# Performance work log

Hardware: AMD Instinct MI355X
Metric: run time of the kernel (lower is better)

Reference implementation:

```python
import jax, jax.numpy as jnp
import numpy as np

B, N, D_IN = 256, 64, 128   # batch, n_agents, input_dim
H0, H1, H2 = 256, 256, 64   # rnn_hidden_dim[0], [1], [2]


def setup_inputs() -> dict:
    key = jax.random.key(0)
    ks = jax.random.split(key, 14)
    s = 0.05
    return {
        "obs": jax.random.normal(ks[0], (B, N, D_IN), dtype=jnp.float32),
        "W_enc": jax.random.normal(ks[1], (H0, D_IN), dtype=jnp.float32) * s,
        "b_enc": jax.random.normal(ks[2], (H0,), dtype=jnp.float32) * s,
        "W_obs": jax.random.normal(ks[3], (H0, H0), dtype=jnp.float32) * s,
        "b_obs": jax.random.normal(ks[4], (H0,), dtype=jnp.float32) * s,
        "W_ih": jax.random.normal(ks[5], (3 * H0, H0), dtype=jnp.float32) * s,
        "b_ih": jax.random.normal(ks[6], (3 * H0,), dtype=jnp.float32) * s,
        "W_hh": jax.random.normal(ks[7], (3 * H0, H0), dtype=jnp.float32) * s,
        "b_hh": jax.random.normal(ks[8], (3 * H0,), dtype=jnp.float32) * s,
        "W_val": jax.random.normal(ks[9], (H1, H0), dtype=jnp.float32) * s,
        "b_val": jax.random.normal(ks[10], (H1,), dtype=jnp.float32) * s,
        "W_dec": jax.random.normal(ks[11], (H2, H1), dtype=jnp.float32) * s,
        "b_dec": jax.random.normal(ks[12], (H2,), dtype=jnp.float32) * s,
    }


def reference(obs, W_enc, b_enc, W_obs, b_obs, W_ih, b_ih, W_hh, b_hh,
              W_val, b_val, W_dec, b_dec):
    # encoding + f_obs  -> h: [B, N, H0]
    x = jax.nn.relu(jnp.einsum("bnd,hd->bnh", obs, W_enc) + b_enc)
    h = jnp.einsum("bnh,gh->bng", x, W_obs) + b_obs

    # comm: mean over other agents. Original masks self and divides by N
    # (mean over dim of size N with self zeroed) => (sum_all - self) / N.
    c = (jnp.sum(h, axis=1, keepdims=True) - h) / N  # [B, N, H0]

    # GRUCell(input=c, hidden=h), PyTorch gate ordering r, z, n
    gi = jnp.einsum("bnh,gh->bng", c, W_ih) + b_ih   # [B, N, 3*H0]
    gh = jnp.einsum("bnh,gh->bng", h, W_hh) + b_hh
    gi_r, gi_z, gi_n = jnp.split(gi, 3, axis=-1)
    gh_r, gh_z, gh_n = jnp.split(gh, 3, axis=-1)
    r = jax.nn.sigmoid(gi_r + gh_r)
    z = jax.nn.sigmoid(gi_z + gh_z)
    n = jnp.tanh(gi_n + r * gh_n)
    h = (1.0 - z) * n + z * h  # [B, N, H0]

    # value head + decoding; seq_len=1 squeezed -> [B, N, H2]
    v = jnp.einsum("bnh,vh->bnv", h, W_val) + b_val
    out = jnp.einsum("bnv,ov->bno", v, W_dec) + b_dec
    return out
```

## Files before the change

kernel.cpp:

```cpp
#include <hip/hip_runtime.h>
#include <hip/hip_bf16.h>
#include <math.h>


typedef __bf16  bf16x8 __attribute__((ext_vector_type(8)));
typedef float   f32x4  __attribute__((ext_vector_type(4)));

#define DIN 128
#define H0  256
#define SW  264
#define SWO 136
#define LOG2E 1.44269504088896f

#define O_WENC 0
#define O_WOBS 32768
#define O_WIH  98304
#define O_WHH  294912
#define O_WVAL 491520
#define O_WDEC 557056
#define W_TOT  573440

__device__ __forceinline__ f32x4 mfma16(bf16x8 a, bf16x8 b, f32x4 c) {
    return __builtin_amdgcn_mfma_f32_16x16x32_bf16(a, b, c, 0, 0, 0);
}
__device__ __forceinline__ float bf2f(__hip_bfloat16 x) { return __bfloat162float(x); }
__device__ __forceinline__ __hip_bfloat16 f2bf(float x) { return __float2bfloat16(x); }

__device__ __forceinline__ float fsigmoid(float x) {
    float e = __builtin_amdgcn_exp2f(-LOG2E * x);
    return __builtin_amdgcn_rcpf(1.0f + e);
}
__device__ __forceinline__ float ftanh(float x) {
    float e = __builtin_amdgcn_exp2f(2.0f * LOG2E * x);
    return 1.0f - 2.0f * __builtin_amdgcn_rcpf(1.0f + e);
}

__device__ __forceinline__ bf16x8 w8(const __hip_bfloat16* p, int idx) {
    return *(const bf16x8*)(p + idx);
}

__device__ __forceinline__ int tadr(int r, int k) { return r * SW + k; }
__device__ __forceinline__ int oadr(int r, int k) { return r * SWO + k; }

__global__ __launch_bounds__(256) void prep_kernel(
    const float* __restrict__ W_enc, const float* __restrict__ W_obs,
    const float* __restrict__ W_ih,  const float* __restrict__ W_hh,
    const float* __restrict__ W_val, const float* __restrict__ W_dec,
    __hip_bfloat16* __restrict__ ws)
{
    const int i = (blockIdx.x * 256 + threadIdx.x) * 8;
    if (i >= W_TOT) return;
    const float* src; int off;
    if      (i < O_WOBS) { src = W_enc; off = O_WENC; }
    else if (i < O_WIH)  { src = W_obs; off = O_WOBS; }
    else if (i < O_WHH)  { src = W_ih;  off = O_WIH;  }
    else if (i < O_WVAL) { src = W_hh;  off = O_WHH;  }
    else if (i < O_WDEC) { src = W_val; off = O_WVAL; }
    else                 { src = W_dec; off = O_WDEC; }
    const float* f = src + (i - off);
    f32x4 a = *(const f32x4*)f;
    f32x4 b = *(const f32x4*)(f + 4);
    bf16x8 v;
    #pragma unroll
    for (int j = 0; j < 4; j++) { v[j] = (__bf16)a[j]; v[j + 4] = (__bf16)b[j]; }
    *(bf16x8*)(ws + i) = v;
}

__global__ __launch_bounds__(512, 2) void commnet_mfma(
    const __hip_bfloat16* __restrict__ ws,
    const float* __restrict__ b_enc, const float* __restrict__ b_obs,
    const float* __restrict__ b_ih,  const float* __restrict__ b_hh,
    const float* __restrict__ b_val, const float* __restrict__ b_dec,
    const float* __restrict__ obs,   float* __restrict__ out)
{
    __shared__ __align__(16) __hip_bfloat16 T0[64 * SW];
    __shared__ __align__(16) __hip_bfloat16 T1[64 * SW];

    const __hip_bfloat16* W_enc = ws + O_WENC;
    const __hip_bfloat16* W_obs = ws + O_WOBS;
    const __hip_bfloat16* W_ih  = ws + O_WIH;
    const __hip_bfloat16* W_hh  = ws + O_WHH;
    const __hip_bfloat16* W_val = ws + O_WVAL;
    const __hip_bfloat16* W_dec = ws + O_WDEC;

    const int tid  = threadIdx.x;
    const int wave = tid >> 6;
    const int lane = tid & 63;
    const int quad = lane >> 4;
    const int lc   = lane & 15;
    const int row0 = blockIdx.x * 64;
    const int ko16 = quad * 8;

    for (int i = tid; i < 64 * DIN / 8; i += 512) {
        const int r = i >> 4;
        const int c = (i & 15) << 3;
        const float* src = obs + (row0 + r) * DIN + c;
        f32x4 a = *(const f32x4*)src;
        f32x4 b = *(const f32x4*)(src + 4);
        bf16x8 v;
        #pragma unroll
        for (int j = 0; j < 4; j++) { v[j] = (__bf16)a[j]; v[j + 4] = (__bf16)b[j]; }
        *(bf16x8*)&T1[oadr(r, c)] = v;
    }
    __syncthreads();

    #pragma unroll
    for (int cp = 0; cp < 2; cp++) {
        const int n = (wave + 8 * cp) * 16 + lc;
        const float bias = b_enc[n];
        f32x4 acc[4] = {};
        #pragma unroll
        for (int k0 = 0; k0 < DIN; k0 += 32) {
            const int kk = k0 + ko16;
            bf16x8 b = w8(W_enc, n * DIN + kk);
            #pragma unroll
            for (int rt = 0; rt < 4; rt++) {
                bf16x8 a = *(const bf16x8*)&T1[oadr(rt * 16 + lc, kk)];
                acc[rt] = mfma16(a, b, acc[rt]);
            }
        }
        #pragma unroll
        for (int rt = 0; rt < 4; rt++)
            #pragma unroll
            for (int i = 0; i < 4; i++) {
                const int row = rt * 16 + quad * 4 + i;
                T0[tadr(row, n)] = f2bf(fmaxf(acc[rt][i] + bias, 0.0f));
            }
    }
    __syncthreads();

    #pragma unroll
    for (int cp = 0; cp < 2; cp++) {
        const int n = (wave + 8 * cp) * 16 + lc;
        const float bias = b_obs[n];
        f32x4 acc[4] = {};
        #pragma unroll 2
        for (int k0 = 0; k0 < H0; k0 += 32) {
            const int kk = k0 + ko16;
            bf16x8 b = w8(W_obs, n * H0 + kk);
            #pragma unroll
            for (int rt = 0; rt < 4; rt++) {
                bf16x8 a = *(const bf16x8*)&T0[tadr(rt * 16 + lc, kk)];
                acc[rt] = mfma16(a, b, acc[rt]);
            }
        }
        #pragma unroll
        for (int rt = 0; rt < 4; rt++)
            #pragma unroll
            for (int i = 0; i < 4; i++) {
                const int row = rt * 16 + quad * 4 + i;
                T1[tadr(row, n)] = f2bf(acc[rt][i] + bias);
            }
    }
    __syncthreads();

    #pragma unroll
    for (int cp = 0; cp < 2; cp++) {
        const int n = (wave + 8 * cp) * 16 + lc;
        const float bir = b_ih[n], biz = b_ih[n + 256], bin = b_ih[n + 512];
        const float bhr = b_hh[n], bhz = b_hh[n + 256], bhn = b_hh[n + 512];
        f32x4 gir[4] = {}, giz[4] = {}, gin[4] = {};
        f32x4 ghr[4] = {}, ghz[4] = {}, ghn[4] = {};
        #pragma unroll 2
        for (int k0 = 0; k0 < H0; k0 += 32) {
            const int kk = k0 + ko16;
            bf16x8 bir8 = w8(W_ih, (n      ) * H0 + kk);
            bf16x8 biz8 = w8(W_ih, (n + 256) * H0 + kk);
            bf16x8 bin8 = w8(W_ih, (n + 512) * H0 + kk);
            bf16x8 bhr8 = w8(W_hh, (n      ) * H0 + kk);
            bf16x8 bhz8 = w8(W_hh, (n + 256) * H0 + kk);
            bf16x8 bhn8 = w8(W_hh, (n + 512) * H0 + kk);
            #pragma unroll
            for (int rt = 0; rt < 4; rt++) {
                bf16x8 aH = *(const bf16x8*)&T1[tadr(rt * 16 + lc, kk)];
                gir[rt] = mfma16(aH, bir8, gir[rt]);
                giz[rt] = mfma16(aH, biz8, giz[rt]);
                gin[rt] = mfma16(aH, bin8, gin[rt]);
                ghr[rt] = mfma16(aH, bhr8, ghr[rt]);
                ghz[rt] = mfma16(aH, bhz8, ghz[rt]);
                ghn[rt] = mfma16(aH, bhn8, ghn[rt]);
            }
        }
        float Sr = 0.0f, Sz = 0.0f, Sn = 0.0f;
        #pragma unroll
        for (int rt = 0; rt < 4; rt++)
            #pragma unroll
            for (int i = 0; i < 4; i++) {
                Sr += gir[rt][i]; Sz += giz[rt][i]; Sn += gin[rt][i];
            }
        Sr += __shfl_xor(Sr, 16); Sr += __shfl_xor(Sr, 32);
        Sz += __shfl_xor(Sz, 16); Sz += __shfl_xor(Sz, 32);
        Sn += __shfl_xor(Sn, 16); Sn += __shfl_xor(Sn, 32);

        #pragma unroll
        for (int rt = 0; rt < 4; rt++)
            #pragma unroll
            for (int i = 0; i < 4; i++) {
                const int row = rt * 16 + quad * 4 + i;
                const float gi_r = (Sr - gir[rt][i]) * (1.0f / 64.0f) + bir;
                const float gi_z = (Sz - giz[rt][i]) * (1.0f / 64.0f) + biz;
                const float gi_n = (Sn - gin[rt][i]) * (1.0f / 64.0f) + bin;
                const float r  = fsigmoid(gi_r + ghr[rt][i] + bhr);
                const float z  = fsigmoid(gi_z + ghz[rt][i] + bhz);
                const float nn = ftanh(gi_n + r * (ghn[rt][i] + bhn));
                const float h  = bf2f(T1[tadr(row, n)]);
                T0[tadr(row, n)] = f2bf((1.0f - z) * nn + z * h);
            }
    }
    __syncthreads();

    #pragma unroll
    for (int cp = 0; cp < 2; cp++) {
        const int n = (wave + 8 * cp) * 16 + lc;
        const float bias = b_val[n];
        f32x4 acc[4] = {};
        #pragma unroll 2
        for (int k0 = 0; k0 < H0; k0 += 32) {
            const int kk = k0 + ko16;
            bf16x8 b = w8(W_val, n * H0 + kk);
            #pragma unroll
            for (int rt = 0; rt < 4; rt++) {
                bf16x8 a = *(const bf16x8*)&T0[tadr(rt * 16 + lc, kk)];
                acc[rt] = mfma16(a, b, acc[rt]);
            }
        }
        #pragma unroll
        for (int rt = 0; rt < 4; rt++)
            #pragma unroll
            for (int i = 0; i < 4; i++) {
                const int row = rt * 16 + quad * 4 + i;
                T1[tadr(row, n)] = f2bf(acc[rt][i] + bias);
            }
    }
    __syncthreads();

    {
        const int ct  = wave & 3;
        const int rtb = (wave >> 2) * 2;
        const int n   = ct * 16 + lc;
        const float bias = b_dec[n];
        f32x4 acc[2] = {};
        #pragma unroll 2
        for (int k0 = 0; k0 < H0; k0 += 32) {
            const int kk = k0 + ko16;
            bf16x8 b = w8(W_dec, n * H0 + kk);
            #pragma unroll
            for (int j = 0; j < 2; j++) {
                bf16x8 a = *(const bf16x8*)&T1[tadr((rtb + j) * 16 + lc, kk)];
                acc[j] = mfma16(a, b, acc[j]);
            }
        }
        #pragma unroll
        for (int j = 0; j < 2; j++)
            #pragma unroll
            for (int i = 0; i < 4; i++) {
                const int row = (rtb + j) * 16 + quad * 4 + i;
                out[(row0 + row) * 64 + n] = acc[j][i] + bias;
            }
    }
}

extern "C" void kernel_launch(void* const* d_in, const int* in_sizes, int n_in,
                              void* d_out, int out_size, void* d_ws, size_t ws_size,
                              hipStream_t stream) {
    (void)in_sizes; (void)n_in; (void)out_size; (void)ws_size;
    const float* obs   = (const float*)d_in[0];
    const float* W_enc = (const float*)d_in[1];  const float* b_enc = (const float*)d_in[2];
    const float* W_obs = (const float*)d_in[3];  const float* b_obs = (const float*)d_in[4];
    const float* W_ih  = (const float*)d_in[5];  const float* b_ih  = (const float*)d_in[6];
    const float* W_hh  = (const float*)d_in[7];  const float* b_hh  = (const float*)d_in[8];
    const float* W_val = (const float*)d_in[9];  const float* b_val = (const float*)d_in[10];
    const float* W_dec = (const float*)d_in[11]; const float* b_dec = (const float*)d_in[12];
    float* out = (float*)d_out;
    __hip_bfloat16* ws = (__hip_bfloat16*)d_ws;

    prep_kernel<<<280, 256, 0, stream>>>(W_enc, W_obs, W_ih, W_hh, W_val, W_dec, ws);
    commnet_mfma<<<256, 512, 0, stream>>>(
        ws, b_enc, b_obs, b_ih, b_hh, b_val, b_dec, obs, out);
}
```

Before: 122.6 us.

## Fold value and decoder layers into one matrix and prefetch weight fragments

Adds a small kernel that precomputes W_dec·W_val and the folded bias, so the main kernel runs one 256→64 GEMM in place of the value GEMM, its barrier and the decoder GEMM. Weight loads in each GEMM loop are software-prefetched one k-step ahead to hide global latency, and the launch bounds drop the two-blocks-per-CU hint. The fold adds an extra serial launch with a naive per-thread dot-product loop. It also changes rounding, since the intermediate v is no longer quantized to bf16.

Result: slower. 134.7 us (+9.9%).

```diff
diff --git a/kernel.cpp b/kernel.cpp
--- a/kernel.cpp
+++ b/kernel.cpp
@@ -16,16 +16,15 @@
 #define O_WOBS 32768
 #define O_WIH  98304
 #define O_WHH  294912
-#define O_WVAL 491520
-#define O_WDEC 557056
-#define W_TOT  573440
+#define W_TOT4 491520
+#define O_WVD  491520
+#define BVD_BYTE 1015808
 
 __device__ __forceinline__ f32x4 mfma16(bf16x8 a, bf16x8 b, f32x4 c) {
     return __builtin_amdgcn_mfma_f32_16x16x32_bf16(a, b, c, 0, 0, 0);
 }
 __device__ __forceinline__ float bf2f(__hip_bfloat16 x) { return __bfloat162float(x); }
 __device__ __forceinline__ __hip_bfloat16 f2bf(float x) { return __float2bfloat16(x); }
-
 __device__ __forceinline__ float fsigmoid(float x) {
     float e = __builtin_amdgcn_exp2f(-LOG2E * x);
     return __builtin_amdgcn_rcpf(1.0f + e);
@@ -34,29 +33,22 @@
     float e = __builtin_amdgcn_exp2f(2.0f * LOG2E * x);
     return 1.0f - 2.0f * __builtin_amdgcn_rcpf(1.0f + e);
 }
-
 __device__ __forceinline__ bf16x8 w8(const __hip_bfloat16* p, int idx) {
     return *(const bf16x8*)(p + idx);
 }
-
-__device__ __forceinline__ int tadr(int r, int k) { return r * SW + k; }
-__device__ __forceinline__ int oadr(int r, int k) { return r * SWO + k; }
 
 __global__ __launch_bounds__(256) void prep_kernel(
     const float* __restrict__ W_enc, const float* __restrict__ W_obs,
     const float* __restrict__ W_ih,  const float* __restrict__ W_hh,
-    const float* __restrict__ W_val, const float* __restrict__ W_dec,
     __hip_bfloat16* __restrict__ ws)
 {
     const int i = (blockIdx.x * 256 + threadIdx.x) * 8;
-    if (i >= W_TOT) return;
+    if (i >= W_TOT4) return;
     const float* src; int off;
     if      (i < O_WOBS) { src = W_enc; off = O_WENC; }
     else if (i < O_WIH)  { src = W_obs; off = O_WOBS; }
     else if (i < O_WHH)  { src = W_ih;  off = O_WIH;  }
-    else if (i < O_WVAL) { src = W_hh;  off = O_WHH;  }
-    else if (i < O_WDEC) { src = W_val; off = O_WVAL; }
-    else                 { src = W_dec; off = O_WDEC; }
+    else                 { src = W_hh;  off = O_WHH;  }
     const float* f = src + (i - off);
     f32x4 a = *(const f32x4*)f;
     f32x4 b = *(const f32x4*)(f + 4);
@@ -66,11 +58,28 @@
     *(bf16x8*)(ws + i) = v;
 }
 
-__global__ __launch_bounds__(512, 2) void commnet_mfma(
-    const __hip_bfloat16* __restrict__ ws,
+__global__ __launch_bounds__(256) void wvd_kernel(
+    const float* __restrict__ W_dec, const float* __restrict__ W_val,
+    const float* __restrict__ b_val, const float* __restrict__ b_dec,
+    __hip_bfloat16* __restrict__ wvd, float* __restrict__ bvd)
+{
+    const int o = blockIdx.x;
+    const int h = threadIdx.x;
+    float acc = 0.0f;
+    for (int v = 0; v < 256; v++)
+        acc += W_dec[o * 256 + v] * W_val[v * 256 + h];
+    wvd[o * 256 + h] = f2bf(acc);
+    if (h == 0) {
+        float b = b_dec[o];
+        for (int v = 0; v < 256; v++) b += W_dec[o * 256 + v] * b_val[v];
+        bvd[o] = b;
+    }
+}
+
+__global__ __launch_bounds__(512, 1) void commnet_v8(
+    const __hip_bfloat16* __restrict__ ws, const float* __restrict__ bvd,
     const float* __restrict__ b_enc, const float* __restrict__ b_obs,
     const float* __restrict__ b_ih,  const float* __restrict__ b_hh,
-    const float* __restrict__ b_val, const float* __restrict__ b_dec,
     const float* __restrict__ obs,   float* __restrict__ out)
 {
     __shared__ __align__(16) __hip_bfloat16 T0[64 * SW];
@@ -80,8 +89,7 @@
     const __hip_bfloat16* W_obs = ws + O_WOBS;
     const __hip_bfloat16* W_ih  = ws + O_WIH;
     const __hip_bfloat16* W_hh  = ws + O_WHH;
-    const __hip_bfloat16* W_val = ws + O_WVAL;
-    const __hip_bfloat16* W_dec = ws + O_WDEC;
+    const __hip_bfloat16* W_vd  = ws + O_WVD;
 
     const int tid  = threadIdx.x;
     const int wave = tid >> 6;
@@ -91,16 +99,17 @@
     const int row0 = blockIdx.x * 64;
     const int ko16 = quad * 8;
 
-    for (int i = tid; i < 64 * DIN / 8; i += 512) {
-        const int r = i >> 4;
-        const int c = (i & 15) << 3;
+    #pragma unroll
+    for (int j = 0; j < 2; j++) {
+        const int u = tid + j * 512;
+        const int r = u >> 4, c = (u & 15) << 3;
         const float* src = obs + (row0 + r) * DIN + c;
         f32x4 a = *(const f32x4*)src;
         f32x4 b = *(const f32x4*)(src + 4);
         bf16x8 v;
         #pragma unroll
-        for (int j = 0; j < 4; j++) { v[j] = (__bf16)a[j]; v[j + 4] = (__bf16)b[j]; }
-        *(bf16x8*)&T1[oadr(r, c)] = v;
+        for (int q = 0; q < 4; q++) { v[q] = (__bf16)a[q]; v[q + 4] = (__bf16)b[q]; }
+        *(bf16x8*)&T1[r * SWO + c] = v;
     }
     __syncthreads();
 
@@ -109,23 +118,23 @@
         const int n = (wave + 8 * cp) * 16 + lc;
         const float bias = b_enc[n];
         f32x4 acc[4] = {};
+        bf16x8 wc = w8(W_enc, n * DIN + ko16);
         #pragma unroll
         for (int k0 = 0; k0 < DIN; k0 += 32) {
-            const int kk = k0 + ko16;
-            bf16x8 b = w8(W_enc, n * DIN + kk);
+            bf16x8 wn = w8(W_enc, n * DIN + (((k0 + 32) & (DIN - 1)) + ko16));
+            const int kk = k0 + ko16;
             #pragma unroll
             for (int rt = 0; rt < 4; rt++) {
-                bf16x8 a = *(const bf16x8*)&T1[oadr(rt * 16 + lc, kk)];
-                acc[rt] = mfma16(a, b, acc[rt]);
-            }
-        }
-        #pragma unroll
-        for (int rt = 0; rt < 4; rt++)
-            #pragma unroll
-            for (int i = 0; i < 4; i++) {
-                const int row = rt * 16 + quad * 4 + i;
-                T0[tadr(row, n)] = f2bf(fmaxf(acc[rt][i] + bias, 0.0f));
-            }
+                bf16x8 a = *(const bf16x8*)&T1[(rt * 16 + lc) * SWO + kk];
+                acc[rt] = mfma16(a, wc, acc[rt]);
+            }
+            wc = wn;
+        }
+        #pragma unroll
+        for (int rt = 0; rt < 4; rt++)
+            #pragma unroll
+            for (int i = 0; i < 4; i++)
+                T0[(rt * 16 + quad * 4 + i) * SW + n] = f2bf(fmaxf(acc[rt][i] + bias, 0.0f));
     }
     __syncthreads();
 
@@ -134,23 +143,23 @@
         const int n = (wave + 8 * cp) * 16 + lc;
         const float bias = b_obs[n];
         f32x4 acc[4] = {};
+        bf16x8 wc = w8(W_obs, n * H0 + ko16);
         #pragma unroll 2
         for (int k0 = 0; k0 < H0; k0 += 32) {
-            const int kk = k0 + ko16;
-            bf16x8 b = w8(W_obs, n * H0 + kk);
+            bf16x8 wn = w8(W_obs, n * H0 + (((k0 + 32) & (H0 - 1)) + ko16));
+            const int kk = k0 + ko16;
             #pragma unroll
             for (int rt = 0; rt < 4; rt++) {
-                bf16x8 a = *(const bf16x8*)&T0[tadr(rt * 16 + lc, kk)];
-                acc[rt] = mfma16(a, b, acc[rt]);
-            }
-        }
-        #pragma unroll
-        for (int rt = 0; rt < 4; rt++)
-            #pragma unroll
-            for (int i = 0; i < 4; i++) {
-                const int row = rt * 16 + quad * 4 + i;
-                T1[tadr(row, n)] = f2bf(acc[rt][i] + bias);
-            }
+                bf16x8 a = *(const bf16x8*)&T0[(rt * 16 + lc) * SW + kk];
+                acc[rt] = mfma16(a, wc, acc[rt]);
+            }
+            wc = wn;
+        }
+        #pragma unroll
+        for (int rt = 0; rt < 4; rt++)
+            #pragma unroll
+            for (int i = 0; i < 4; i++)
+                T1[(rt * 16 + quad * 4 + i) * SW + n] = f2bf(acc[rt][i] + bias);
     }
     __syncthreads();
 
@@ -161,25 +170,33 @@
         const float bhr = b_hh[n], bhz = b_hh[n + 256], bhn = b_hh[n + 512];
         f32x4 gir[4] = {}, giz[4] = {}, gin[4] = {};
         f32x4 ghr[4] = {}, ghz[4] = {}, ghn[4] = {};
+        bf16x8 c0 = w8(W_ih, (n      ) * H0 + ko16);
+        bf16x8 c1 = w8(W_ih, (n + 256) * H0 + ko16);
+        bf16x8 c2 = w8(W_ih, (n + 512) * H0 + ko16);
+        bf16x8 c3 = w8(W_hh, (n      ) * H0 + ko16);
+        bf16x8 c4 = w8(W_hh, (n + 256) * H0 + ko16);
+        bf16x8 c5 = w8(W_hh, (n + 512) * H0 + ko16);
         #pragma unroll 2
         for (int k0 = 0; k0 < H0; k0 += 32) {
-            const int kk = k0 + ko16;
-            bf16x8 bir8 = w8(W_ih, (n      ) * H0 + kk);
-            bf16x8 biz8 = w8(W_ih, (n + 256) * H0 + kk);
-            bf16x8 bin8 = w8(W_ih, (n + 512) * H0 + kk);
-            bf16x8 bhr8 = w8(W_hh, (n      ) * H0 + kk);
-            bf16x8 bhz8 = w8(W_hh, (n + 256) * H0 + kk);
-            bf16x8 bhn8 = w8(W_hh, (n + 512) * H0 + kk);
+            const int kn = ((k0 + 32) & (H0 - 1)) + ko16;
+            bf16x8 d0 = w8(W_ih, (n      ) * H0 + kn);
+            bf16x8 d1 = w8(W_ih, (n + 256) * H0 + kn);
+            bf16x8 d2 = w8(W_ih, (n + 512) * H0 + kn);
+            bf16x8 d3 = w8(W_hh, (n      ) * H0 + kn);
+            bf16x8 d4 = w8(W_hh, (n + 256) * H0 + kn);
+            bf16x8 d5 = w8(W_hh, (n + 512) * H0 + kn);
+            const int kk = k0 + ko16;
             #pragma unroll
             for (int rt = 0; rt < 4; rt++) {
-                bf16x8 aH = *(const bf16x8*)&T1[tadr(rt * 16 + lc, kk)];
-                gir[rt] = mfma16(aH, bir8, gir[rt]);
-                giz[rt] = mfma16(aH, biz8, giz[rt]);
-                gin[rt] = mfma16(aH, bin8, gin[rt]);
-                ghr[rt] = mfma16(aH, bhr8, ghr[rt]);
-                ghz[rt] = mfma16(aH, bhz8, ghz[rt]);
-                ghn[rt] = mfma16(aH, bhn8, ghn[rt]);
-            }
+                bf16x8 aH = *(const bf16x8*)&T1[(rt * 16 + lc) * SW + kk];
+                gir[rt] = mfma16(aH, c0, gir[rt]);
+                giz[rt] = mfma16(aH, c1, giz[rt]);
+                gin[rt] = mfma16(aH, c2, gin[rt]);
+                ghr[rt] = mfma16(aH, c3, ghr[rt]);
+                ghz[rt] = mfma16(aH, c4, ghz[rt]);
+                ghn[rt] = mfma16(aH, c5, ghn[rt]);
+            }
+            c0 = d0; c1 = d1; c2 = d2; c3 = d3; c4 = d4; c5 = d5;
         }
         float Sr = 0.0f, Sz = 0.0f, Sn = 0.0f;
         #pragma unroll
@@ -191,7 +208,6 @@
         Sr += __shfl_xor(Sr, 16); Sr += __shfl_xor(Sr, 32);
         Sz += __shfl_xor(Sz, 16); Sz += __shfl_xor(Sz, 32);
         Sn += __shfl_xor(Sn, 16); Sn += __shfl_xor(Sn, 32);
-
         #pragma unroll
         for (int rt = 0; rt < 4; rt++)
             #pragma unroll
@@ -203,33 +219,8 @@
                 const float r  = fsigmoid(gi_r + ghr[rt][i] + bhr);
                 const float z  = fsigmoid(gi_z + ghz[rt][i] + bhz);
                 const float nn = ftanh(gi_n + r * (ghn[rt][i] + bhn));
-                const float h  = bf2f(T1[tadr(row, n)]);
-                T0[tadr(row, n)] = f2bf((1.0f - z) * nn + z * h);
-            }
-    }
-    __syncthreads();
-
-    #pragma unroll
-    for (int cp = 0; cp < 2; cp++) {
-        const int n = (wave + 8 * cp) * 16 + lc;
-        const float bias = b_val[n];
-        f32x4 acc[4] = {};
-        #pragma unroll 2
-        for (int k0 = 0; k0 < H0; k0 += 32) {
-            const int kk = k0 + ko16;
-            bf16x8 b = w8(W_val, n * H0 + kk);
-            #pragma unroll
-            for (int rt = 0; rt < 4; rt++) {
-                bf16x8 a = *(const bf16x8*)&T0[tadr(rt * 16 + lc, kk)];
-                acc[rt] = mfma16(a, b, acc[rt]);
-            }
-        }
-        #pragma unroll
-        for (int rt = 0; rt < 4; rt++)
-            #pragma unroll
-            for (int i = 0; i < 4; i++) {
-                const int row = rt * 16 + quad * 4 + i;
-                T1[tadr(row, n)] = f2bf(acc[rt][i] + bias);
+                const float h  = bf2f(T1[row * SW + n]);
+                T0[row * SW + n] = f2bf((1.0f - z) * nn + z * h);
             }
     }
     __syncthreads();
@@ -238,17 +229,19 @@
         const int ct  = wave & 3;
         const int rtb = (wave >> 2) * 2;
         const int n   = ct * 16 + lc;
-        const float bias = b_dec[n];
+        const float bias = bvd[n];
         f32x4 acc[2] = {};
-        #pragma unroll 2
+        bf16x8 wc = w8(W_vd, n * H0 + ko16);
+        #pragma unroll
         for (int k0 = 0; k0 < H0; k0 += 32) {
-            const int kk = k0 + ko16;
-            bf16x8 b = w8(W_dec, n * H0 + kk);
+            bf16x8 wn = w8(W_vd, n * H0 + (((k0 + 32) & (H0 - 1)) + ko16));
+            const int kk = k0 + ko16;
             #pragma unroll
             for (int j = 0; j < 2; j++) {
-                bf16x8 a = *(const bf16x8*)&T1[tadr((rtb + j) * 16 + lc, kk)];
-                acc[j] = mfma16(a, b, acc[j]);
-            }
+                bf16x8 a = *(const bf16x8*)&T0[((rtb + j) * 16 + lc) * SW + kk];
+                acc[j] = mfma16(a, wc, acc[j]);
+            }
+            wc = wn;
         }
         #pragma unroll
         for (int j = 0; j < 2; j++)
@@ -273,8 +266,9 @@
     const float* W_dec = (const float*)d_in[11]; const float* b_dec = (const float*)d_in[12];
     float* out = (float*)d_out;
     __hip_bfloat16* ws = (__hip_bfloat16*)d_ws;
-
-    prep_kernel<<<280, 256, 0, stream>>>(W_enc, W_obs, W_ih, W_hh, W_val, W_dec, ws);
-    commnet_mfma<<<256, 512, 0, stream>>>(
-        ws, b_enc, b_obs, b_ih, b_hh, b_val, b_dec, obs, out);
-}
+    float* bvd = (float*)((char*)d_ws + BVD_BYTE);
+
+    prep_kernel<<<240, 256, 0, stream>>>(W_enc, W_obs, W_ih, W_hh, ws);
+    wvd_kernel<<<64, 256, 0, stream>>>(W_dec, W_val, b_val, b_dec, ws + O_WVD, bvd);
+    commnet_v8<<<256, 512, 0, stream>>>(ws, bvd, b_enc, b_obs, b_ih, b_hh, obs, out);
+}
```
